# Kernel tuning notes

Measured on AMD Instinct MI355X. Metric: run time of the kernel, lower is better.

Reference implementation:

```python
import jax, jax.numpy as jnp
import numpy as np

B, IN_C, L, D, K, DEPTH, OUT = 16, 3, 2048, 256, 8, 4, 1
F = L // 2 + 1
EPS = 1e-5


def _hilbert_basis_rfft(grid_size, k):
    # Hilbert matrix Z[i,j] = 1/(i+j+1), symmetric PSD; take top-k eigvecs.
    i = np.arange(grid_size, dtype=np.float64)
    Z = 1.0 / (i[:, None] + i[None, :] + 1.0)
    w, V = np.linalg.eigh(Z)
    idx = np.argsort(w)[::-1][:k]
    Vt = V.T[idx]                                   # (k, L)
    Phi_f = np.fft.rfft(Vt, n=grid_size, axis=-1)   # (k, L//2+1) complex
    return Phi_f.astype(np.complex64)


def setup_inputs() -> dict:
    key = jax.random.key(0)
    ks = jax.random.split(key, 10)
    phi = _hilbert_basis_rfft(L, K)
    s = 0.05
    return {
        "x": jax.random.normal(ks[0], (B, IN_C, L), jnp.float32),
        "lift_w": jax.random.normal(ks[1], (D, IN_C + 1), jnp.float32) * s,
        "lift_b": jax.random.normal(ks[2], (D,), jnp.float32) * s,
        "theta": jax.random.normal(ks[3], (DEPTH, K, D, D), jnp.float32) * (1.0 / np.sqrt(D)),
        "ln_gamma": jnp.ones((DEPTH, D), jnp.float32),
        "ln_beta": jnp.zeros((DEPTH, D), jnp.float32),
        "glu_val_w": jax.random.normal(ks[4], (DEPTH, D, D), jnp.float32) * (1.0 / np.sqrt(D)),
        "glu_val_b": jax.random.normal(ks[5], (DEPTH, D), jnp.float32) * s,
        "glu_gate_w": jax.random.normal(ks[6], (DEPTH, D, D), jnp.float32) * (1.0 / np.sqrt(D)),
        "glu_gate_b": jax.random.normal(ks[7], (DEPTH, D), jnp.float32) * s,
        "head_w": jax.random.normal(ks[8], (OUT, D), jnp.float32) * (1.0 / np.sqrt(D)),
        "head_b": jax.random.normal(ks[9], (OUT,), jnp.float32) * s,
        "phi_real": jnp.asarray(phi.real, jnp.float32),
        "phi_imag": jnp.asarray(phi.imag, jnp.float32),
    }


def _layernorm_channels(h, gamma, beta):
    # h: (b, d, t); normalize over channel dim d (matches LayerNorm on transposed input)
    mu = jnp.mean(h, axis=1, keepdims=True)
    var = jnp.mean(jnp.square(h - mu), axis=1, keepdims=True)
    z = (h - mu) * jax.lax.rsqrt(var + EPS)
    return z * gamma[None, :, None] + beta[None, :, None]


def reference(x, lift_w, lift_b, theta, ln_gamma, ln_beta,
              glu_val_w, glu_val_b, glu_gate_w, glu_gate_b,
              head_w, head_b, phi_real, phi_imag):
    phi = phi_real + 1j * phi_imag                      # (K, F) complex
    phi_c = jnp.conj(phi)
    # add grid coordinate channel
    coords = jnp.linspace(0.0, 1.0, L, dtype=x.dtype)
    coords = jnp.broadcast_to(coords[None, None, :], (x.shape[0], 1, L))
    h = jnp.concatenate([x, coords], axis=1)            # (b, in+1, L)
    # pointwise lift (Conv1d kernel_size=1, norm=Identity)
    h = jnp.einsum("oi,bit->bot", lift_w, h) + lift_b[None, :, None]
    for i in range(DEPTH):
        z = _layernorm_channels(h, ln_gamma[i], ln_beta[i])
        Xf = jnp.fft.rfft(z, axis=-1)                   # (b, d, F) complex64
        # Exploit FFT linearity: S = sum_{l,d} Theta[l,h,d] * irfft(Xf[b,d] * conj(Phi[l]))
        #                          = irfft( sum_{l,d} Theta[l,h,d]*conj(Phi[l,f]) * Xf[b,d,f] )
        W = jnp.einsum("lhd,lf->hdf", theta[i].astype(Xf.dtype), phi_c)  # (h, d, F)
        Sf = jnp.einsum("bdf,hdf->bhf", Xf, W)          # (b, h, F)
        S = jnp.fft.irfft(Sf, n=L, axis=-1)             # (b, h, L)
        V = jnp.einsum("od,bdt->bot", glu_val_w[i], S) + glu_val_b[i][None, :, None]
        G = jax.nn.sigmoid(jnp.einsum("od,bdt->bot", glu_gate_w[i], S) + glu_gate_b[i][None, :, None])
        h = h + V * G                                   # residual + GLU
    y = jnp.einsum("od,bdt->bot", head_w, h) + head_b[None, :, None]
    return y
```

## Files before the change

### kernel.cpp

```cpp
#include <hip/hip_runtime.h>
#include <math.h>

#define NB 16
#define CIN 3
#define LL 2048
#define DD 256
#define KK 8
#define NDEPTH 4
#define FF 1025
#define FFP 1032
#define FFS 1032
#define LOGL 11

typedef _Float16 half8 __attribute__((ext_vector_type(8)));
typedef _Float16 half2v __attribute__((ext_vector_type(2)));
typedef float f32x4 __attribute__((ext_vector_type(4)));

union H8 { half8 h8; unsigned int u[4]; uint4 q; };
union H2 { _Float16 h[2]; unsigned int u; half2v v; };
union PK4 { float2 f2[4]; uint4 q[2]; };

#if defined(__has_builtin)
#if __has_builtin(__builtin_amdgcn_fdot2)
#define HAS_FDOT2 1
#endif
#endif

__device__ inline float fdot2_acc(unsigned int a, unsigned int b, float c){
    H2 ua, ub; ua.u = a; ub.u = b;
#ifdef HAS_FDOT2
    return __builtin_amdgcn_fdot2(ua.v, ub.v, c, false);
#else
    return c + (float)ua.h[0]*(float)ub.h[0] + (float)ua.h[1]*(float)ub.h[1];
#endif
}

__device__ inline float2 cmul(const float2 a, const float2 b){
    return make_float2(a.x*b.x - a.y*b.y, a.x*b.y + a.y*b.x);
}
__device__ inline float2 cadd(const float2 a, const float2 b){ return make_float2(a.x+b.x, a.y+b.y); }
__device__ inline float2 csub(const float2 a, const float2 b){ return make_float2(a.x-b.x, a.y-b.y); }

template<bool CONJ>
__device__ inline void r8_stage(float2* a, const float2* __restrict__ tw, int g, int s){
    const int hs = 1 << s;
    int pos = g & (hs-1);
    int grp = g >> s;
    int q = (grp << (s+3)) + pos;
    float2 ws = tw[pos << (LOGL-1-s)];
    float2 w1 = tw[pos << (LOGL-2-s)];
    float2 w2 = tw[(pos+hs) << (LOGL-2-s)];
    float2 v0 = tw[pos << (LOGL-3-s)];
    float2 v1 = tw[(pos+hs) << (LOGL-3-s)];
    float2 v2 = tw[(pos+2*hs) << (LOGL-3-s)];
    float2 v3 = tw[(pos+3*hs) << (LOGL-3-s)];
    if (CONJ){ ws.y=-ws.y; w1.y=-w1.y; w2.y=-w2.y; v0.y=-v0.y; v1.y=-v1.y; v2.y=-v2.y; v3.y=-v3.y; }
    float2 A0=a[q],      A1=a[q+hs],   A2=a[q+2*hs], A3=a[q+3*hs],
           A4=a[q+4*hs], A5=a[q+5*hs], A6=a[q+6*hs], A7=a[q+7*hs];
    float2 t;
    t=cmul(ws,A1); float2 b0=cadd(A0,t), b1=csub(A0,t);
    t=cmul(ws,A3); float2 b2=cadd(A2,t), b3=csub(A2,t);
    t=cmul(ws,A5); float2 b4=cadd(A4,t), b5=csub(A4,t);
    t=cmul(ws,A7); float2 b6=cadd(A6,t), b7=csub(A6,t);
    t=cmul(w1,b2); float2 c0=cadd(b0,t), c2=csub(b0,t);
    t=cmul(w2,b3); float2 c1=cadd(b1,t), c3=csub(b1,t);
    t=cmul(w1,b6); float2 c4=cadd(b4,t), c6=csub(b4,t);
    t=cmul(w2,b7); float2 c5=cadd(b5,t), c7=csub(b5,t);
    t=cmul(v0,c4); a[q]      =cadd(c0,t); a[q+4*hs]=csub(c0,t);
    t=cmul(v1,c5); a[q+hs]   =cadd(c1,t); a[q+5*hs]=csub(c1,t);
    t=cmul(v2,c6); a[q+2*hs] =cadd(c2,t); a[q+6*hs]=csub(c2,t);
    t=cmul(v3,c7); a[q+3*hs] =cadd(c3,t); a[q+7*hs]=csub(c3,t);
}

template<bool CONJ>
__device__ inline void r4_final(float2* a, const float2* __restrict__ tw, int g){
    int pos = g;
    float2 ws = tw[pos << 1];
    float2 w1 = tw[pos];
    float2 w2 = tw[pos + 512];
    if (CONJ){ ws.y=-ws.y; w1.y=-w1.y; w2.y=-w2.y; }
    float2 a0 = a[pos], a1 = a[pos+512], a2 = a[pos+1024], a3 = a[pos+1536];
    float2 t1 = cmul(ws, a1), t3 = cmul(ws, a3);
    float2 x0 = cadd(a0,t1), x1 = csub(a0,t1);
    float2 x2 = cadd(a2,t3), x3 = csub(a2,t3);
    float2 u1 = cmul(w1, x2), u2 = cmul(w2, x3);
    a[pos]      = cadd(x0,u1);
    a[pos+1024] = csub(x0,u1);
    a[pos+512]  = cadd(x1,u2);
    a[pos+1536] = csub(x1,u2);
}

__global__ void twiddle_kernel(float2* __restrict__ tw){
    int j = blockIdx.x*blockDim.x + threadIdx.x;
    if (j < LL/2){
        double ang = -2.0*3.14159265358979323846*(double)j/(double)LL;
        tw[j] = make_float2((float)cos(ang), (float)sin(ang));
    }
}

__global__ void conv_w_kernel(const float* __restrict__ wv, const float* __restrict__ wg,
                              _Float16* __restrict__ Wf){
    int idx = blockIdx.x*256 + threadIdx.x;
    int layer = idx >> 17;
    int vg = (idx >> 16) & 1;
    int rem = idx & 65535;
    int o = rem >> 8, d = rem & 255;
    const float* src = (vg ? wg : wv) + ((size_t)layer << 16);
    float val = src[(o << 8) + d];
    size_t dst = ((((size_t)(layer*2+vg)*16 + (o>>4))*8 + (d>>5))*64
                  + (o&15) + 16*((d>>3)&3))*8 + (d&7);
    Wf[dst] = (_Float16)val;
}

__global__ void transpose_theta16_kernel(const float* __restrict__ in,
                                         unsigned int* __restrict__ out){
    __shared__ float tile[2][32][33];
    int m = blockIdx.z;
    int layer = m >> 2, lp = m & 3;
    int d0 = blockIdx.x*32, h0 = blockIdx.y*32;
    int tx = threadIdx.x & 31, ty = threadIdx.x >> 5;
    const float* src0 = in + ((size_t)layer*KK + 2*lp)*DD*DD;
    const float* src1 = src0 + (size_t)DD*DD;
    #pragma unroll
    for (int i = 0; i < 4; ++i){
        tile[0][ty + i*8][tx] = src0[(size_t)(h0 + ty + i*8)*DD + d0 + tx];
        tile[1][ty + i*8][tx] = src1[(size_t)(h0 + ty + i*8)*DD + d0 + tx];
    }
    __syncthreads();
    #pragma unroll
    for (int i = 0; i < 4; ++i){
        H2 p;
        p.h[0] = (_Float16)tile[0][tx][ty + i*8];
        p.h[1] = (_Float16)tile[1][tx][ty + i*8];
        out[((size_t)m*DD + d0 + ty + i*8)*DD + h0 + tx] = p.u;
    }
}

__global__ __launch_bounds__(256) void lift_ln_kernel(const float* __restrict__ x,
        const float* __restrict__ lw, const float* __restrict__ lb,
        const float* __restrict__ gamma, const float* __restrict__ beta,
        float* __restrict__ h, _Float16* __restrict__ z){
    __shared__ float red[2][4][64];
    __shared__ float stat[2][64];
    __shared__ float gb[512];
    int tid = threadIdx.x;
    int t = tid & 63, dg = tid >> 6;
    int b = blockIdx.y;
    int tg = blockIdx.x*64 + t;
    gb[tid] = gamma[tid];
    gb[256 + tid] = beta[tid];
    const float* xb = x + (size_t)b*CIN*LL;
    float x0 = xb[tg], x1 = xb[LL + tg], x2 = xb[2*LL + tg];
    float coord = (float)tg * (1.0f/(LL-1));
    float hv[64];
    float s = 0.f, ss = 0.f;
    float* hp = h + (size_t)b*DD*LL + tg;
    #pragma unroll
    for (int j = 0; j < 64; ++j){
        int d = dg*64 + j;
        float4 w = *(const float4*)&lw[d*4];
        float v = lb[d];
        v = fmaf(w.x, x0, v); v = fmaf(w.y, x1, v);
        v = fmaf(w.z, x2, v); v = fmaf(w.w, coord, v);
        hv[j] = v;
        s += v; ss = fmaf(v, v, ss);
        hp[(size_t)d*LL] = v;
    }
    red[0][dg][t] = s; red[1][dg][t] = ss;
    __syncthreads();
    if (tid < 64){
        float S1 = red[0][0][tid] + red[0][1][tid] + red[0][2][tid] + red[0][3][tid];
        float S2 = red[1][0][tid] + red[1][1][tid] + red[1][2][tid] + red[1][3][tid];
        float mu = S1*(1.0f/DD);
        float var = S2*(1.0f/DD) - mu*mu;
        stat[0][tid] = mu;
        stat[1][tid] = rsqrtf(var + 1e-5f);
    }
    __syncthreads();
    float mu = stat[0][t], rs = stat[1][t];
    _Float16* zp = z + (size_t)b*DD*LL + tg;
    #pragma unroll
    for (int j = 0; j < 64; ++j){
        int d = dg*64 + j;
        zp[(size_t)d*LL] = (_Float16)((hv[j] - mu)*rs*gb[d] + gb[256 + d]);
    }
}

__global__ __launch_bounds__(256) void fft_fwd_pair_kernel(const unsigned int* __restrict__ zh,
                                                           unsigned int* __restrict__ XfH,
                                                           const float2* __restrict__ tw){
    __shared__ float2 a[LL];
    int blk = blockIdx.x;
    const unsigned int* s0 = zh + (size_t)(blk*2)*(LL/2);
    const unsigned int* s1 = s0 + (LL/2);
    int tid = threadIdx.x;
    #pragma unroll
    for (int i = 0; i < 4; ++i){
        int tp = tid + i*256;
        H2 u0, u1;
        u0.u = s0[tp];
        u1.u = s1[tp];
        int t0 = 2*tp, t1 = 2*tp + 1;
        int r0 = __brev((unsigned)t0) >> (32-LOGL);
        int r1 = __brev((unsigned)t1) >> (32-LOGL);
        a[r0] = make_float2((float)u0.h[0], (float)u1.h[0]);
        a[r1] = make_float2((float)u0.h[1], (float)u1.h[1]);
    }
    __syncthreads();
    r8_stage<false>(a, tw, tid, 0);  __syncthreads();
    r8_stage<false>(a, tw, tid, 3);  __syncthreads();
    r8_stage<false>(a, tw, tid, 6);  __syncthreads();
    r4_final<false>(a, tw, tid);
    r4_final<false>(a, tw, tid + 256);
    __syncthreads();
    unsigned int* dst0 = XfH + (size_t)(blk*2)*FFP;
    unsigned int* dst1 = dst0 + FFP;
    #pragma unroll
    for (int i = 0; i < 5; ++i){
        int f = tid + i*256;
        if (f <= 1024){
            int m = (LL - f) & (LL-1);
            float2 A = a[f], B = a[m];
            H2 p0, p1;
            p0.h[0] = (_Float16)(0.5f*(A.x + B.x));
            p0.h[1] = (_Float16)(0.5f*(A.y - B.y));
            p1.h[0] = (_Float16)(0.5f*(A.y + B.y));
            p1.h[1] = (_Float16)(0.5f*(B.x - A.x));
            dst0[f] = p0.u;
            dst1[f] = p1.u;
        }
    }
    if (tid < 7){
        dst0[1025 + tid] = 0u;
        dst1[1025 + tid] = 0u;
    }
}

__global__ __launch_bounds__(256) void fft_inv_pair_kernel(const float2* __restrict__ Sf0,
                                                           unsigned int* __restrict__ Sfrag,
                                                           const float2* __restrict__ tw){
    __shared__ float2 a[LL];
    int blk = blockIdx.x;
    const float2* src0 = Sf0 + (size_t)(blk*2)*FFS;
    const float2* src1 = src0 + FFS;
    int tid = threadIdx.x;
    #pragma unroll
    for (int i = 0; i < LL/256; ++i){
        int idx = tid + i*256;
        float2 Y;
        if (idx <= 1024){
            float2 s0 = src0[idx], s1 = src1[idx];
            Y = make_float2(s0.x - s1.y, s0.y + s1.x);
        } else {
            int m = LL - idx;
            float2 s0 = src0[m], s1 = src1[m];
            Y = make_float2(s0.x + s1.y, s1.x - s0.y);
        }
        int rev = __brev((unsigned)idx) >> (32-LOGL);
        a[rev] = Y;
    }
    __syncthreads();
    r8_stage<true>(a, tw, tid, 0);  __syncthreads();
    r8_stage<true>(a, tw, tid, 3);  __syncthreads();
    r8_stage<true>(a, tw, tid, 6);  __syncthreads();
    r4_final<true>(a, tw, tid);
    r4_final<true>(a, tw, tid + 256);
    __syncthreads();
    int b = blk >> 7, dl = (blk & 127)*2;
    int kc = dl >> 5, lq4 = (dl >> 3) & 3, jh = (dl & 7) >> 1;
    unsigned int* dst = Sfrag + ((size_t)(b*8 + kc)*128)*64*4;
    const float sc = 1.0f/(float)LL;
    #pragma unroll
    for (int i = 0; i < LL/256; ++i){
        int t = tid + i*256;
        float2 v = a[t];
        H2 p;
        p.h[0] = (_Float16)(v.x*sc);
        p.h[1] = (_Float16)(v.y*sc);
        dst[(((t>>4)*64) + (t&15) + 16*lq4)*4 + jh] = p.u;
    }
}

__global__ __launch_bounds__(512, 4) void spectral7_kernel(
    const unsigned int* __restrict__ XfH,
    const unsigned int* __restrict__ th16,
    const float* __restrict__ phr, const float* __restrict__ phim,
    float2* __restrict__ Sf0){
    __shared__ unsigned int Apairs[8*64*8];
    __shared__ unsigned int phi2[2][8][4];
    int tid = threadIdx.x;
    int w = tid >> 6, lane = tid & 63;
    int hc = w & 3, fh = w >> 2;
    int n = lane & 15, kp = lane >> 4;
    int f0 = blockIdx.x * 8;
    int h0 = blockIdx.y * 64;
    int h = h0 + hc*16 + n;

    if (tid < 32){
        int ff = tid >> 2, lp = tid & 3;
        H2 a, b;
        a.h[0] = (_Float16)phr[(2*lp)*FF + f0 + ff];
        a.h[1] = (_Float16)phr[(2*lp+1)*FF + f0 + ff];
        b.h[0] = (_Float16)(-phim[(2*lp)*FF + f0 + ff]);
        b.h[1] = (_Float16)(-phim[(2*lp+1)*FF + f0 + ff]);
        phi2[0][ff][lp] = a.u;
        phi2[1][ff][lp] = b.u;
    }

    f32x4 accre[4], accim[4];
    #pragma unroll
    for (int i = 0; i < 4; ++i){
        accre[i] = (f32x4){0.f,0.f,0.f,0.f};
        accim[i] = (f32x4){0.f,0.f,0.f,0.f};
    }

    for (int kc = 0; kc < 8; ++kc){
        unsigned int th_pk[4][8];
        #pragma unroll
        for (int lp = 0; lp < 4; ++lp)
            #pragma unroll
            for (int j = 0; j < 8; ++j)
                th_pk[lp][j] = th16[((size_t)lp*DD + kc*32 + kp*8 + j)*DD + h];

        __syncthreads();
        {
            int bb = tid & 15;
            int dd = tid >> 4;
            const uint4* src = (const uint4*)(XfH + ((size_t)(bb*DD + kc*32 + dd)*FFP + f0));
            uint4 v0 = src[0], v1 = src[1];
            int L = bb + 16*(dd >> 3), j = dd & 7;
            unsigned int vv[8] = {v0.x, v0.y, v0.z, v0.w, v1.x, v1.y, v1.z, v1.w};
            #pragma unroll
            for (int ff = 0; ff < 8; ++ff){
                int A = ff*2048 + L*32 + j*4;
                int sw = (((A >> 7) & 3) << 5) | (((A >> 8) & 1) << 4);
                *(unsigned int*)((char*)Apairs + (A ^ sw)) = vv[ff];
            }
        }
        __syncthreads();

        #pragma unroll
        for (int ffl = 0; ffl < 4; ++ffl){
            int ff = fh*4 + ffl;
            unsigned int pr2[4], pi2[4];
            #pragma unroll
            for (int lp = 0; lp < 4; ++lp){
                pr2[lp] = phi2[0][ff][lp];
                pi2[lp] = phi2[1][ff][lp];
            }
            int Ab = ff*2048 + lane*32;
            int sw = (((Ab >> 7) & 3) << 5) | (((Ab >> 8) & 1) << 4);
            Ab ^= sw;
            uint4 lo = *(const uint4*)((const char*)Apairs + Ab);
            uint4 hi = *(const uint4*)((const char*)Apairs + (Ab ^ 16));
            unsigned int dw[8] = {lo.x, lo.y, lo.z, lo.w, hi.x, hi.y, hi.z, hi.w};
            H8 Are, Aim, Anim;
            #pragma unroll
            for (int k = 0; k < 4; ++k){
                Are.u[k]  = __builtin_amdgcn_perm(dw[2*k+1], dw[2*k], 0x05040100u);
                Aim.u[k]  = __builtin_amdgcn_perm(dw[2*k+1], dw[2*k], 0x07060302u);
                Anim.u[k] = Aim.u[k] ^ 0x80008000u;
            }
            float wre[8], wim[8];
            #pragma unroll
            for (int j = 0; j < 8; ++j){
                float re = 0.f, im = 0.f;
                #pragma unroll
                for (int lp = 0; lp < 4; ++lp){
                    re = fdot2_acc(th_pk[lp][j], pr2[lp], re);
                    im = fdot2_acc(th_pk[lp][j], pi2[lp], im);
                }
                wre[j] = re; wim[j] = im;
            }
            H8 Bre, Bim;
            #pragma unroll
            for (int j = 0; j < 8; ++j){
                Bre.h8[j] = (_Float16)wre[j];
                Bim.h8[j] = (_Float16)wim[j];
            }
            accre[ffl] = __builtin_amdgcn_mfma_f32_16x16x32_f16(Are.h8,  Bre.h8, accre[ffl], 0, 0, 0);
            accre[ffl] = __builtin_amdgcn_mfma_f32_16x16x32_f16(Anim.h8, Bim.h8, accre[ffl], 0, 0, 0);
            accim[ffl] = __builtin_amdgcn_mfma_f32_16x16x32_f16(Are.h8,  Bim.h8, accim[ffl], 0, 0, 0);
            accim[ffl] = __builtin_amdgcn_mfma_f32_16x16x32_f16(Aim.h8,  Bre.h8, accim[ffl], 0, 0, 0);
        }
    }
    #pragma unroll
    for (int r = 0; r < 4; ++r){
        int bb = kp*4 + r;
        PK4 pk;
        #pragma unroll
        for (int ffl = 0; ffl < 4; ++ffl)
            pk.f2[ffl] = make_float2(accre[ffl][r], accim[ffl][r]);
        uint4* dst = (uint4*)(Sf0 + ((size_t)(bb*DD) + h)*FFS + f0 + fh*4);
        dst[0] = pk.q[0]; dst[1] = pk.q[1];
    }
}

__global__ __launch_bounds__(256) void nyq_kernel(const unsigned int* __restrict__ XfH,
    const unsigned int* __restrict__ th16,
    const float* __restrict__ phr, const float* __restrict__ phim,
    float2* __restrict__ Sf0){
    __shared__ float2 red[256];
    int tid = threadIdx.x;
    int hb = blockIdx.x, b = blockIdx.y;
    int h = hb*16 + (tid & 15);
    int dp = tid >> 4;
    float pr[KK], pi[KK];
    #pragma unroll
    for (int l = 0; l < KK; ++l){ pr[l] = phr[l*FF + 1024]; pi[l] = -phim[l*FF + 1024]; }
    float2 acc = make_float2(0.f, 0.f);
    for (int j = 0; j < 16; ++j){
        int d = dp*16 + j;
        float wre = 0.f, wim = 0.f;
        #pragma unroll
        for (int lp = 0; lp < 4; ++lp){
            H2 t; t.u = th16[((size_t)lp*DD + d)*DD + h];
            float t0 = (float)t.h[0], t1 = (float)t.h[1];
            wre = fmaf(t0, pr[2*lp], fmaf(t1, pr[2*lp+1], wre));
            wim = fmaf(t0, pi[2*lp], fmaf(t1, pi[2*lp+1], wim));
        }
        H2 u; u.u = XfH[(size_t)(b*DD + d)*FFP + 1024];
        float2 x = make_float2((float)u.h[0], (float)u.h[1]);
        acc.x = fmaf(x.x, wre, fmaf(-x.y, wim, acc.x));
        acc.y = fmaf(x.x, wim, fmaf( x.y, wre, acc.y));
    }
    red[tid] = acc;
    __syncthreads();
    if (tid < 16){
        float2 s = make_float2(0.f, 0.f);
        #pragma unroll
        for (int k = 0; k < 16; ++k){ s.x += red[tid + k*16].x; s.y += red[tid + k*16].y; }
        Sf0[((size_t)b*DD + hb*16 + tid)*FFS + 1024] = s;
    }
}

template<int MODE>
__global__ __launch_bounds__(256, 2) void glu_mfma_kernel(
    const uint4* __restrict__ Sfrag,
    const uint4* __restrict__ WfL,
    const float* __restrict__ bv, const float* __restrict__ bg,
    float* __restrict__ h, float* __restrict__ outp,
    const float* __restrict__ aux1, const float* __restrict__ aux2){
    __shared__ float sb[1024];
    __shared__ float red[2][4][4][16];
    __shared__ float stat[2][4][16];
    int tid = threadIdx.x;
    int w = tid >> 6, lane = tid & 63;
    int tl = lane & 15, lq = lane >> 4;
    int b = blockIdx.y, tb4 = blockIdx.x;

    sb[tid] = bv[tid];
    sb[256 + tid] = bg[tid];
    sb[512 + tid] = aux1[tid];
    if (MODE == 0) sb[768 + tid] = aux2[tid];
    __syncthreads();

    f32x4 aV[4][4], aG[4][4];
    #pragma unroll
    for (int mt = 0; mt < 4; ++mt)
        #pragma unroll
        for (int nt = 0; nt < 4; ++nt){
            aV[mt][nt] = (f32x4){0.f,0.f,0.f,0.f};
            aG[mt][nt] = (f32x4){0.f,0.f,0.f,0.f};
        }

    for (int kc = 0; kc < 8; ++kc){
        H8 Bf[4];
        #pragma unroll
        for (int nt = 0; nt < 4; ++nt)
            Bf[nt].q = Sfrag[((size_t)(b*8 + kc)*128 + tb4*4 + nt)*64 + lane];
        H8 Av[4], Ag[4];
        #pragma unroll
        for (int mt = 0; mt < 4; ++mt){
            int ot = w*4 + mt;
            Av[mt].q = WfL[((size_t)(ot)*8 + kc)*64 + lane];
            Ag[mt].q = WfL[((size_t)(16 + ot)*8 + kc)*64 + lane];
        }
        #pragma unroll
        for (int mt = 0; mt < 4; ++mt)
            #pragma unroll
            for (int nt = 0; nt < 4; ++nt){
                aV[mt][nt] = __builtin_amdgcn_mfma_f32_16x16x32_f16(Av[mt].h8, Bf[nt].h8, aV[mt][nt], 0, 0, 0);
                aG[mt][nt] = __builtin_amdgcn_mfma_f32_16x16x32_f16(Ag[mt].h8, Bf[nt].h8, aG[mt][nt], 0, 0, 0);
            }
    }

    #pragma unroll
    for (int mt = 0; mt < 4; ++mt){
        #pragma unroll
        for (int r = 0; r < 4; ++r){
            int o = w*64 + mt*16 + lq*4 + r;
            float bvv = sb[o], bgv = sb[256 + o];
            float* hp = h + ((size_t)(b*DD + o))*LL + tb4*64 + tl;
            #pragma unroll
            for (int nt = 0; nt < 4; ++nt){
                float v = aV[mt][nt][r] + bvv;
                float g = aG[mt][nt][r] + bgv;
                g = 1.0f/(1.0f + __expf(-g));
                float cur = hp[nt*16] + v*g;
                if (MODE == 0) hp[nt*16] = cur;
                aV[mt][nt][r] = cur;
            }
        }
    }

    float s[4], ss[4];
    #pragma unroll
    for (int nt = 0; nt < 4; ++nt){ s[nt] = 0.f; ss[nt] = 0.f; }
    #pragma unroll
    for (int mt = 0; mt < 4; ++mt)
        #pragma unroll
        for (int r = 0; r < 4; ++r){
            int o = w*64 + mt*16 + lq*4 + r;
            float wo = (MODE == 0) ? 1.0f : sb[512 + o];
            #pragma unroll
            for (int nt = 0; nt < 4; ++nt){
                float cur = aV[mt][nt][r];
                if (MODE == 0){ s[nt] += cur; ss[nt] = fmaf(cur, cur, ss[nt]); }
                else { s[nt] = fmaf(wo, cur, s[nt]); }
            }
        }
    #pragma unroll
    for (int nt = 0; nt < 4; ++nt){
        s[nt] += __shfl_xor(s[nt], 16); s[nt] += __shfl_xor(s[nt], 32);
        if (MODE == 0){ ss[nt] += __shfl_xor(ss[nt], 16); ss[nt] += __shfl_xor(ss[nt], 32); }
    }
    if (lq == 0){
        #pragma unroll
        for (int nt = 0; nt < 4; ++nt){
            red[0][w][nt][tl] = s[nt];
            if (MODE == 0) red[1][w][nt][tl] = ss[nt];
        }
    }
    __syncthreads();
    if (MODE == 0){
        if (tid < 64){
            int nt = tid >> 4, t2 = tid & 15;
            float S1 = red[0][0][nt][t2] + red[0][1][nt][t2] + red[0][2][nt][t2] + red[0][3][nt][t2];
            float S2 = red[1][0][nt][t2] + red[1][1][nt][t2] + red[1][2][nt][t2] + red[1][3][nt][t2];
            float mu = S1*(1.0f/DD);
            float var = S2*(1.0f/DD) - mu*mu;
            stat[0][nt][t2] = mu;
            stat[1][nt][t2] = rsqrtf(var + 1e-5f);
        }
        __syncthreads();
        #pragma unroll
        for (int mt = 0; mt < 4; ++mt){
            #pragma unroll
            for (int r = 0; r < 4; ++r){
                int o = w*64 + mt*16 + lq*4 + r;
                float gam = sb[512 + o], bet = sb[768 + o];
                _Float16* zp = (_Float16*)outp + ((size_t)(b*DD + o))*LL + tb4*64 + tl;
                #pragma unroll
                for (int nt = 0; nt < 4; ++nt){
                    float zv = (aV[mt][nt][r] - stat[0][nt][tl])*stat[1][nt][tl]*gam + bet;
                    zp[nt*16] = (_Float16)zv;
                }
            }
        }
    } else {
        if (tid < 64){
            int nt = tid >> 4, t2 = tid & 15;
            float S1 = red[0][0][nt][t2] + red[0][1][nt][t2] + red[0][2][nt][t2] + red[0][3][nt][t2];
            outp[(size_t)b*LL + tb4*64 + tid] = S1 + aux2[0];
        }
    }
}

extern "C" void kernel_launch(void* const* d_in, const int* in_sizes, int n_in,
                              void* d_out, int out_size, void* d_ws, size_t ws_size,
                              hipStream_t stream){
    (void)in_sizes; (void)n_in; (void)out_size; (void)ws_size;
    const float* x      = (const float*)d_in[0];
    const float* lift_w = (const float*)d_in[1];
    const float* lift_b = (const float*)d_in[2];
    const float* theta  = (const float*)d_in[3];
    const float* ln_g   = (const float*)d_in[4];
    const float* ln_b   = (const float*)d_in[5];
    const float* gvw    = (const float*)d_in[6];
    const float* gvb    = (const float*)d_in[7];
    const float* ggw    = (const float*)d_in[8];
    const float* ggb    = (const float*)d_in[9];
    const float* hw     = (const float*)d_in[10];
    const float* hb     = (const float*)d_in[11];
    const float* phr    = (const float*)d_in[12];
    const float* phim   = (const float*)d_in[13];
    float* out = (float*)d_out;

    char* ws = (char*)d_ws;
    size_t off = 0;
    float2* tw  = (float2*)(ws + off); off += (size_t)(LL/2)*sizeof(float2);
    _Float16* Wf = (_Float16*)(ws + off); off += (size_t)NDEPTH*2*DD*DD*2;
    unsigned int* th16 = (unsigned int*)(ws + off); off += (size_t)NDEPTH*4*DD*DD*4;
    off = (off + 255) & ~(size_t)255;
    float*  h   = (float*)(ws + off);  off += (size_t)NB*DD*LL*4;
    _Float16* zh = (_Float16*)(ws + off); off += (size_t)NB*DD*LL*2;
    unsigned int* XfH = (unsigned int*)(ws + off); off += (size_t)NB*DD*FFP*4;
    unsigned int* Sfrag = XfH;
    off = (off + 255) & ~(size_t)255;
    float2* Sf0 = (float2*)(ws + off); off += (size_t)NB*DD*FFS*8;

    twiddle_kernel<<<4, 256, 0, stream>>>(tw);
    conv_w_kernel<<<(NDEPTH*2*DD*DD)/256, 256, 0, stream>>>(gvw, ggw, Wf);
    transpose_theta16_kernel<<<dim3(8,8,NDEPTH*4), 256, 0, stream>>>(theta, th16);
    lift_ln_kernel<<<dim3(LL/64, NB), 256, 0, stream>>>(x, lift_w, lift_b, ln_g, ln_b, h, zh);

    for (int layer = 0; layer < NDEPTH; ++layer){
        const unsigned int* thL = th16 + (size_t)layer*4*DD*DD;
        const uint4* WfL = (const uint4*)(Wf + (size_t)layer*2*DD*DD);
        fft_fwd_pair_kernel<<<NB*DD/2, 256, 0, stream>>>((const unsigned int*)zh, XfH, tw);
        spectral7_kernel<<<dim3(128,4), 512, 0, stream>>>(XfH, thL, phr, phim, Sf0);
        nyq_kernel<<<dim3(16,16), 256, 0, stream>>>(XfH, thL, phr, phim, Sf0);
        fft_inv_pair_kernel<<<NB*DD/2, 256, 0, stream>>>(Sf0, Sfrag, tw);
        if (layer < NDEPTH-1){
            glu_mfma_kernel<0><<<dim3(LL/64, NB), 256, 0, stream>>>(
                (const uint4*)Sfrag, WfL,
                gvb + layer*DD, ggb + layer*DD, h, (float*)zh,
                ln_g + (layer+1)*DD, ln_b + (layer+1)*DD);
        } else {
            glu_mfma_kernel<1><<<dim3(LL/64, NB), 256, 0, stream>>>(
                (const uint4*)Sfrag, WfL,
                gvb + layer*DD, ggb + layer*DD, h, out, hw, hb);
        }
    }
}
```

Baseline: 525.0 us.

## Double-buffer spectral LDS tiles and store theta untransposed for vector loads

The spectral kernel now double-buffers the Xf tile in shared memory. It prefetches the next d-chunk while computing the current one, which removes one barrier per iteration. Theta is no longer transposed. It is packed in its natural (h,d) order, so each lane can fetch its 8 consecutive d-values with two 16-byte loads instead of eight strided scalar loads. The cost is doubled LDS use and higher register pressure from the fully unrolled loop, which may hurt occupancy under launch_bounds(512,4).

```diff
diff --git a/kernel.cpp b/kernel.cpp
--- a/kernel.cpp
+++ b/kernel.cpp
@@ -112,28 +112,18 @@
     Wf[dst] = (_Float16)val;
 }
 
-__global__ void transpose_theta16_kernel(const float* __restrict__ in,
-                                         unsigned int* __restrict__ out){
-    __shared__ float tile[2][32][33];
-    int m = blockIdx.z;
+__global__ void pack_theta16_kernel(const float* __restrict__ in,
+                                    unsigned int* __restrict__ out){
+    int idx = blockIdx.x*256 + threadIdx.x;
+    int m = idx >> 16;
+    int rem = idx & 65535;
     int layer = m >> 2, lp = m & 3;
-    int d0 = blockIdx.x*32, h0 = blockIdx.y*32;
-    int tx = threadIdx.x & 31, ty = threadIdx.x >> 5;
-    const float* src0 = in + ((size_t)layer*KK + 2*lp)*DD*DD;
-    const float* src1 = src0 + (size_t)DD*DD;
-    #pragma unroll
-    for (int i = 0; i < 4; ++i){
-        tile[0][ty + i*8][tx] = src0[(size_t)(h0 + ty + i*8)*DD + d0 + tx];
-        tile[1][ty + i*8][tx] = src1[(size_t)(h0 + ty + i*8)*DD + d0 + tx];
-    }
-    __syncthreads();
-    #pragma unroll
-    for (int i = 0; i < 4; ++i){
-        H2 p;
-        p.h[0] = (_Float16)tile[0][tx][ty + i*8];
-        p.h[1] = (_Float16)tile[1][tx][ty + i*8];
-        out[((size_t)m*DD + d0 + ty + i*8)*DD + h0 + tx] = p.u;
-    }
+    const float* s0 = in + ((size_t)layer*KK + 2*lp)*DD*DD;
+    const float* s1 = s0 + (size_t)DD*DD;
+    H2 p;
+    p.h[0] = (_Float16)s0[rem];
+    p.h[1] = (_Float16)s1[rem];
+    out[((size_t)m << 16) + rem] = p.u;
 }
 
 __global__ __launch_bounds__(256) void lift_ln_kernel(const float* __restrict__ x,
@@ -281,12 +271,12 @@
     }
 }
 
-__global__ __launch_bounds__(512, 4) void spectral7_kernel(
+__global__ __launch_bounds__(512, 4) void spectral10_kernel(
     const unsigned int* __restrict__ XfH,
     const unsigned int* __restrict__ th16,
     const float* __restrict__ phr, const float* __restrict__ phim,
     float2* __restrict__ Sf0){
-    __shared__ unsigned int Apairs[8*64*8];
+    __shared__ unsigned int Apairs[2][4096];
     __shared__ unsigned int phi2[2][8][4];
     int tid = threadIdx.x;
     int w = tid >> 6, lane = tid & 63;
@@ -307,6 +297,10 @@
         phi2[1][ff][lp] = b.u;
     }
 
+    int sbb = tid & 15;
+    int sdd = tid >> 4;
+    int sL = sbb + 16*(sdd >> 3), sj = sdd & 7;
+
     f32x4 accre[4], accim[4];
     #pragma unroll
     for (int i = 0; i < 4; ++i){
@@ -314,31 +308,41 @@
         accim[i] = (f32x4){0.f,0.f,0.f,0.f};
     }
 
+    {
+        const uint4* src = (const uint4*)(XfH + ((size_t)(sbb*DD + sdd)*FFP + f0));
+        uint4 v0 = src[0], v1 = src[1];
+        unsigned int vv[8] = {v0.x, v0.y, v0.z, v0.w, v1.x, v1.y, v1.z, v1.w};
+        #pragma unroll
+        for (int ff = 0; ff < 8; ++ff){
+            int A = ff*2048 + sL*32 + sj*4;
+            int sw = (((A >> 7) & 3) << 5) | (((A >> 8) & 1) << 4);
+            *(unsigned int*)((char*)Apairs[0] + (A ^ sw)) = vv[ff];
+        }
+    }
+    __syncthreads();
+
+    #pragma unroll
     for (int kc = 0; kc < 8; ++kc){
         unsigned int th_pk[4][8];
         #pragma unroll
-        for (int lp = 0; lp < 4; ++lp)
-            #pragma unroll
-            for (int j = 0; j < 8; ++j)
-                th_pk[lp][j] = th16[((size_t)lp*DD + kc*32 + kp*8 + j)*DD + h];
-
-        __syncthreads();
-        {
-            int bb = tid & 15;
-            int dd = tid >> 4;
-            const uint4* src = (const uint4*)(XfH + ((size_t)(bb*DD + kc*32 + dd)*FFP + f0));
+        for (int lp = 0; lp < 4; ++lp){
+            const uint4* tp = (const uint4*)(th16 + ((size_t)lp*DD + h)*DD + kc*32 + kp*8);
+            uint4 ta = tp[0], tb = tp[1];
+            th_pk[lp][0]=ta.x; th_pk[lp][1]=ta.y; th_pk[lp][2]=ta.z; th_pk[lp][3]=ta.w;
+            th_pk[lp][4]=tb.x; th_pk[lp][5]=tb.y; th_pk[lp][6]=tb.z; th_pk[lp][7]=tb.w;
+        }
+        if (kc < 7){
+            const uint4* src = (const uint4*)(XfH + ((size_t)(sbb*DD + (kc+1)*32 + sdd)*FFP + f0));
             uint4 v0 = src[0], v1 = src[1];
-            int L = bb + 16*(dd >> 3), j = dd & 7;
             unsigned int vv[8] = {v0.x, v0.y, v0.z, v0.w, v1.x, v1.y, v1.z, v1.w};
             #pragma unroll
             for (int ff = 0; ff < 8; ++ff){
-                int A = ff*2048 + L*32 + j*4;
+                int A = ff*2048 + sL*32 + sj*4;
                 int sw = (((A >> 7) & 3) << 5) | (((A >> 8) & 1) << 4);
-                *(unsigned int*)((char*)Apairs + (A ^ sw)) = vv[ff];
-            }
-        }
-        __syncthreads();
-
+                *(unsigned int*)((char*)Apairs[(kc+1)&1] + (A ^ sw)) = vv[ff];
+            }
+        }
+        const char* bufc = (const char*)Apairs[kc & 1];
         #pragma unroll
         for (int ffl = 0; ffl < 4; ++ffl){
             int ff = fh*4 + ffl;
@@ -351,8 +355,8 @@
             int Ab = ff*2048 + lane*32;
             int sw = (((Ab >> 7) & 3) << 5) | (((Ab >> 8) & 1) << 4);
             Ab ^= sw;
-            uint4 lo = *(const uint4*)((const char*)Apairs + Ab);
-            uint4 hi = *(const uint4*)((const char*)Apairs + (Ab ^ 16));
+            uint4 lo = *(const uint4*)(bufc + Ab);
+            uint4 hi = *(const uint4*)(bufc + (Ab ^ 16));
             unsigned int dw[8] = {lo.x, lo.y, lo.z, lo.w, hi.x, hi.y, hi.z, hi.w};
             H8 Are, Aim, Anim;
             #pragma unroll
@@ -383,6 +387,7 @@
             accim[ffl] = __builtin_amdgcn_mfma_f32_16x16x32_f16(Are.h8,  Bim.h8, accim[ffl], 0, 0, 0);
             accim[ffl] = __builtin_amdgcn_mfma_f32_16x16x32_f16(Aim.h8,  Bre.h8, accim[ffl], 0, 0, 0);
         }
+        if (kc < 7) __syncthreads();
     }
     #pragma unroll
     for (int r = 0; r < 4; ++r){
@@ -414,7 +419,7 @@
         float wre = 0.f, wim = 0.f;
         #pragma unroll
         for (int lp = 0; lp < 4; ++lp){
-            H2 t; t.u = th16[((size_t)lp*DD + d)*DD + h];
+            H2 t; t.u = th16[((size_t)lp*DD + h)*DD + d];
             float t0 = (float)t.h[0], t1 = (float)t.h[1];
             wre = fmaf(t0, pr[2*lp], fmaf(t1, pr[2*lp+1], wre));
             wim = fmaf(t0, pi[2*lp], fmaf(t1, pi[2*lp+1], wim));
@@ -602,14 +607,14 @@
 
     twiddle_kernel<<<4, 256, 0, stream>>>(tw);
     conv_w_kernel<<<(NDEPTH*2*DD*DD)/256, 256, 0, stream>>>(gvw, ggw, Wf);
-    transpose_theta16_kernel<<<dim3(8,8,NDEPTH*4), 256, 0, stream>>>(theta, th16);
+    pack_theta16_kernel<<<(NDEPTH*4*DD*DD)/256, 256, 0, stream>>>(theta, th16);
     lift_ln_kernel<<<dim3(LL/64, NB), 256, 0, stream>>>(x, lift_w, lift_b, ln_g, ln_b, h, zh);
 
     for (int layer = 0; layer < NDEPTH; ++layer){
         const unsigned int* thL = th16 + (size_t)layer*4*DD*DD;
         const uint4* WfL = (const uint4*)(Wf + (size_t)layer*2*DD*DD);
         fft_fwd_pair_kernel<<<NB*DD/2, 256, 0, stream>>>((const unsigned int*)zh, XfH, tw);
-        spectral7_kernel<<<dim3(128,4), 512, 0, stream>>>(XfH, thL, phr, phim, Sf0);
+        spectral10_kernel<<<dim3(128,4), 512, 0, stream>>>(XfH, thL, phr, phim, Sf0);
         nyq_kernel<<<dim3(16,16), 256, 0, stream>>>(XfH, thL, phr, phim, Sf0);
         fft_inv_pair_kernel<<<NB*DD/2, 256, 0, stream>>>(Sf0, Sfrag, tw);
         if (layer < NDEPTH-1){
```

Result: slower. 585.7 us (+11.5%).
